# Performance work log

Hardware: AMD Instinct MI355X
Metric: run time of the kernel (lower is better)

Reference implementation:

```python
import jax, jax.numpy as jnp
import numpy as np

B, S, H = 1, 2048, 1024
E, INTER, TOP_K = 8, 2048, 2
ALPHA, LIMIT = 1.702, 7.0


def setup_inputs() -> dict:
    key = jax.random.key(0)
    ks = jax.random.split(key, 7)
    sc = 0.02
    return {
        'hidden_states': jax.random.normal(ks[0], (B, S, H), jnp.float32),
        'router_w': jax.random.normal(ks[1], (H, E), jnp.float32) * sc,
        'router_b': jax.random.normal(ks[2], (E,), jnp.float32) * sc,
        'gate_up_proj': jax.random.normal(ks[3], (E, H, 2 * INTER), jnp.float32) * sc,
        'gate_up_bias': jax.random.normal(ks[4], (E, 2 * INTER), jnp.float32) * sc,
        'down_proj': jax.random.normal(ks[5], (E, INTER, H), jnp.float32) * sc,
        'down_bias': jax.random.normal(ks[6], (E, H), jnp.float32) * sc,
    }


def reference(hidden_states, router_w, router_b, gate_up_proj, gate_up_bias, down_proj, down_bias):
    x = hidden_states  # [B,S,H]
    # router: top-k over expert logits, softmax over selected logits (gpt-oss style)
    logits = jnp.einsum('bsh,he->bse', x, router_w) + router_b
    top_vals, top_idx = jax.lax.top_k(logits, TOP_K)          # [B,S,K]
    topk_weights = jax.nn.softmax(top_vals, axis=-1)          # [B,S,K]
    # dense per-expert gate_up GEMM (dispatch is identity on 1 device)
    gu = jnp.einsum('bsh,ehn->besn', x, gate_up_proj)         # [B,E,S,2I]
    gu = gu + gate_up_bias[None, :, None, :]
    gate = jnp.minimum(gu[..., :INTER], LIMIT)
    up = jnp.clip(gu[..., INTER:], -LIMIT, LIMIT)
    glu = gate * jax.nn.sigmoid(gate * ALPHA)
    act = (up + 1.0) * glu                                    # [B,E,S,I]
    down = jnp.einsum('besl,elh->besh', act, down_proj)       # [B,E,S,H]
    down = down + down_bias[None, :, None, :]
    # combine: gather each token's K selected expert outputs, weight and sum
    down_bseh = jnp.transpose(down, (0, 2, 1, 3))             # [B,S,E,H]
    idx = jnp.broadcast_to(top_idx[..., None], (B, S, TOP_K, H))
    sel = jnp.take_along_axis(down_bseh, idx, axis=2)         # [B,S,K,H]
    return (sel * topk_weights[..., None]).sum(axis=2)        # [B,S,H]
```

## Files before the change

### kernel.cpp

```cpp
#include <hip/hip_runtime.h>
#include <hip/hip_bf16.h>
#include <math.h>

#define S 2048
#define H 1024
#define NE 8
#define INTER 2048
#define ALPHA 1.702f
#define LIMIT 7.0f

typedef __bf16 bf16x8 __attribute__((ext_vector_type(8)));
typedef float f32x4 __attribute__((ext_vector_type(4)));
typedef unsigned short u16x8 __attribute__((ext_vector_type(8)));

#define WS_COUNTS 0
#define WS_SLOTS  4096
#define WS_W      (WS_SLOTS + NE*S*4)
#define WS_XB     (WS_W + 2*S*4)
#define WS_GUP    (WS_XB + (size_t)S*H*2)
#define WS_DPN    (WS_GUP + (size_t)NE*2*INTER*H*2)
#define WS_ACT    (WS_DPN + (size_t)NE*H*INTER*2)

static __device__ __forceinline__ unsigned short f2bf(float f) {
    union { __hip_bfloat16 h; unsigned short u; } cv;
    cv.h = __float2bfloat16(f);
    return cv.u;
}

static __device__ __forceinline__ void gload16(const void* g, void* l) {
    __builtin_amdgcn_global_load_lds(
        (const __attribute__((address_space(1))) unsigned int*)(unsigned long long)g,
        (__attribute__((address_space(3))) unsigned int*)(unsigned int)(unsigned long long)l,
        16, 0, 0);
}

__global__ __launch_bounds__(64) void router_conv(
    const float* __restrict__ x, const float* __restrict__ rw,
    const float* __restrict__ rb, int* __restrict__ counts,
    int* __restrict__ slots, float* __restrict__ slot_w,
    unsigned short* __restrict__ xb)
{
    int tok = blockIdx.x;
    int lane = threadIdx.x;
    const float4* xr = (const float4*)(x + (size_t)tok * H);
    ushort4* xo = (ushort4*)(xb + (size_t)tok * H);
    float acc[NE];
#pragma unroll
    for (int e = 0; e < NE; ++e) acc[e] = 0.f;
#pragma unroll
    for (int p = 0; p < H / 256; ++p) {
        int idx = p * 64 + lane;
        float4 v = xr[idx];
        ushort4 o;
        o.x = f2bf(v.x); o.y = f2bf(v.y); o.z = f2bf(v.z); o.w = f2bf(v.w);
        xo[idx] = o;
        const float* wr = rw + (size_t)idx * 4 * NE;
#pragma unroll
        for (int e = 0; e < NE; ++e)
            acc[e] += v.x * wr[e] + v.y * wr[NE + e] + v.z * wr[2 * NE + e] + v.w * wr[3 * NE + e];
    }
#pragma unroll
    for (int e = 0; e < NE; ++e) {
#pragma unroll
        for (int off = 32; off > 0; off >>= 1)
            acc[e] += __shfl_down(acc[e], off);
    }
    if (lane == 0) {
        float v[NE];
#pragma unroll
        for (int e = 0; e < NE; ++e) v[e] = acc[e] + rb[e];
        int i1 = 0; float v1 = v[0];
#pragma unroll
        for (int e = 1; e < NE; ++e) if (v[e] > v1) { v1 = v[e]; i1 = e; }
        int i2 = -1; float v2 = -3.0e38f;
#pragma unroll
        for (int e = 0; e < NE; ++e) if (e != i1 && v[e] > v2) { v2 = v[e]; i2 = e; }
        float w1 = 1.f / (1.f + expf(v2 - v1));
        float w2 = 1.f - w1;
        int p1 = atomicAdd(&counts[i1], 1);
        slots[i1 * S + p1] = tok * 2;
        slot_w[tok * 2] = w1;
        int p2 = atomicAdd(&counts[i2], 1);
        slots[i2 * S + p2] = tok * 2 + 1;
        slot_w[tok * 2 + 1] = w2;
    }
}

__global__ __launch_bounds__(256) void prep(
    const float* __restrict__ gup, const float* __restrict__ dp,
    unsigned short* __restrict__ gw, unsigned short* __restrict__ dw)
{
    int z = blockIdx.y;
    int e = z / 3, which = z % 3;
    const float* in;
    unsigned short* out;
    int K, N, istride;
    if (which == 0) {
        in = gup + (size_t)e * H * 2 * INTER;
        out = gw + (size_t)e * 2 * INTER * H;
        K = H; N = INTER; istride = 2 * INTER;
    } else if (which == 1) {
        in = gup + (size_t)e * H * 2 * INTER + INTER;
        out = gw + (size_t)e * 2 * INTER * H + (size_t)INTER * H;
        K = H; N = INTER; istride = 2 * INTER;
    } else {
        in = dp + (size_t)e * INTER * H;
        out = dw + (size_t)e * H * INTER;
        K = INTER; N = H; istride = H;
    }
    int ntiles = N / 64;
    int k0 = (blockIdx.x / ntiles) * 64;
    int n0 = (blockIdx.x % ntiles) * 64;

    __shared__ unsigned short tile[64][68];
    int t = threadIdx.x;
    int lk = t >> 4, ln = (t & 15) * 4;
#pragma unroll
    for (int p = 0; p < 4; ++p) {
        int kk = lk + p * 16;
        float4 v = *(const float4*)(in + (size_t)(k0 + kk) * istride + n0 + ln);
        ushort4 o;
        o.x = f2bf(v.x); o.y = f2bf(v.y); o.z = f2bf(v.z); o.w = f2bf(v.w);
        *(ushort4*)&tile[kk][ln] = o;
    }
    __syncthreads();
    int wn = t >> 3, wk = (t & 7) * 8;
#pragma unroll
    for (int p = 0; p < 2; ++p) {
        int nn = wn + p * 32;
        u16x8 o;
#pragma unroll
        for (int i = 0; i < 8; ++i) o[i] = tile[wk + i][nn];
        *(u16x8*)(out + (size_t)(n0 + nn) * K + k0 + wk) = o;
    }
}

__global__ __launch_bounds__(256) void gateup_mfma(
    const unsigned short* __restrict__ xb,
    const unsigned short* __restrict__ gw,
    const float* __restrict__ gub,
    const int* __restrict__ counts, const int* __restrict__ slots,
    unsigned short* __restrict__ act)
{
    int e = blockIdx.z;
    int cnt = counts[e];
    int m0 = blockIdx.y * 128;
    if (m0 >= cnt) return;
    int n0 = blockIdx.x * 64;

    __shared__ unsigned short As[128 * 32];
    __shared__ unsigned short Gs[64 * 32];
    __shared__ unsigned short Us[64 * 32];
    __shared__ int sl[128];

    int t = threadIdx.x;
    int lane = t & 63, w = t >> 6;
    if (t < 128) {
        int r = m0 + t;
        sl[t] = slots[e * S + (r < cnt ? r : cnt - 1)];
    }
    __syncthreads();

    int quad = lane >> 4, l16 = lane & 15;
    int wm = (w >> 1) * 64, wn = (w & 1) * 32;

    int ar0 = w * 32 + (lane >> 2);
    int ar1 = ar0 + 16;
    const unsigned short* ap0 = xb + (size_t)(sl[ar0] >> 1) * H + (lane & 3) * 8;
    const unsigned short* ap1 = xb + (size_t)(sl[ar1] >> 1) * H + (lane & 3) * 8;
    int bn = w * 16 + (lane >> 2);
    const unsigned short* gp = gw + (size_t)e * 2 * INTER * H + (size_t)(n0 + bn) * H + (lane & 3) * 8;
    const unsigned short* up = gp + (size_t)INTER * H;

    unsigned short* la0 = &As[(2 * w) * 512 + lane * 8];
    unsigned short* la1 = &As[(2 * w + 1) * 512 + lane * 8];
    unsigned short* lg = &Gs[w * 512 + lane * 8];
    unsigned short* lu = &Us[w * 512 + lane * 8];

    f32x4 accg[4][2], accu[4][2];
#pragma unroll
    for (int mi = 0; mi < 4; ++mi)
#pragma unroll
        for (int ni = 0; ni < 2; ++ni) {
            accg[mi][ni] = (f32x4){0.f, 0.f, 0.f, 0.f};
            accu[mi][ni] = (f32x4){0.f, 0.f, 0.f, 0.f};
        }

    for (int k0 = 0; k0 < H; k0 += 32) {
        __syncthreads();
        gload16(ap0 + k0, la0);
        gload16(ap1 + k0, la1);
        gload16(gp + k0, lg);
        gload16(up + k0, lu);
        __syncthreads();
        bf16x8 af[4], gf[2], uf[2];
#pragma unroll
        for (int mi = 0; mi < 4; ++mi)
            af[mi] = *(const bf16x8*)&As[(wm + mi * 16 + l16) * 32 + quad * 8];
#pragma unroll
        for (int ni = 0; ni < 2; ++ni) {
            gf[ni] = *(const bf16x8*)&Gs[(wn + ni * 16 + l16) * 32 + quad * 8];
            uf[ni] = *(const bf16x8*)&Us[(wn + ni * 16 + l16) * 32 + quad * 8];
        }
#pragma unroll
        for (int mi = 0; mi < 4; ++mi)
#pragma unroll
            for (int ni = 0; ni < 2; ++ni) {
                accg[mi][ni] = __builtin_amdgcn_mfma_f32_16x16x32_bf16(af[mi], gf[ni], accg[mi][ni], 0, 0, 0);
                accu[mi][ni] = __builtin_amdgcn_mfma_f32_16x16x32_bf16(af[mi], uf[ni], accu[mi][ni], 0, 0, 0);
            }
    }

    const float* gb = gub + (size_t)e * 2 * INTER;
#pragma unroll
    for (int mi = 0; mi < 4; ++mi) {
#pragma unroll
        for (int r = 0; r < 4; ++r) {
            int rt = wm + mi * 16 + quad * 4 + r;
            if (m0 + rt >= cnt) continue;
            int slot = sl[rt];
            unsigned short* orow = act + (size_t)slot * INTER;
#pragma unroll
            for (int ni = 0; ni < 2; ++ni) {
                int col = n0 + wn + ni * 16 + l16;
                float gate = accg[mi][ni][r] + gb[col];
                float uv = accu[mi][ni][r] + gb[INTER + col];
                gate = fminf(gate, LIMIT);
                uv = fminf(fmaxf(uv, -LIMIT), LIMIT);
                float glu = gate / (1.f + __expf(-ALPHA * gate));
                orow[col] = f2bf((uv + 1.f) * glu);
            }
        }
    }
}

__global__ __launch_bounds__(256) void down_mfma(
    const unsigned short* __restrict__ act,
    const unsigned short* __restrict__ dw,
    const float* __restrict__ db,
    const int* __restrict__ counts, const int* __restrict__ slots,
    const float* __restrict__ slot_w,
    float* __restrict__ out)
{
    int e = blockIdx.z >> 1;
    int ks = blockIdx.z & 1;
    int cnt = counts[e];
    int m0 = blockIdx.y * 128;
    if (m0 >= cnt) return;
    int n0 = blockIdx.x * 64;

    __shared__ unsigned short As[128 * 32];
    __shared__ unsigned short Bs[64 * 32];
    __shared__ int sl[128];

    int t = threadIdx.x;
    int lane = t & 63, w = t >> 6;
    if (t < 128) {
        int r = m0 + t;
        sl[t] = slots[e * S + (r < cnt ? r : cnt - 1)];
    }
    __syncthreads();

    int quad = lane >> 4, l16 = lane & 15;
    int wm = (w >> 1) * 64, wn = (w & 1) * 32;

    int ar0 = w * 32 + (lane >> 2);
    int ar1 = ar0 + 16;
    int kbase = ks * (INTER / 2);
    const unsigned short* ap0 = act + (size_t)sl[ar0] * INTER + kbase + (lane & 3) * 8;
    const unsigned short* ap1 = act + (size_t)sl[ar1] * INTER + kbase + (lane & 3) * 8;
    int bn = w * 16 + (lane >> 2);
    const unsigned short* bp = dw + (size_t)e * H * INTER + (size_t)(n0 + bn) * INTER + kbase + (lane & 3) * 8;

    unsigned short* la0 = &As[(2 * w) * 512 + lane * 8];
    unsigned short* la1 = &As[(2 * w + 1) * 512 + lane * 8];
    unsigned short* lb = &Bs[w * 512 + lane * 8];

    f32x4 acc[4][2];
#pragma unroll
    for (int mi = 0; mi < 4; ++mi)
#pragma unroll
        for (int ni = 0; ni < 2; ++ni)
            acc[mi][ni] = (f32x4){0.f, 0.f, 0.f, 0.f};

    for (int k0 = 0; k0 < INTER / 2; k0 += 32) {
        __syncthreads();
        gload16(ap0 + k0, la0);
        gload16(ap1 + k0, la1);
        gload16(bp + k0, lb);
        __syncthreads();
        bf16x8 af[4], bf[2];
#pragma unroll
        for (int mi = 0; mi < 4; ++mi)
            af[mi] = *(const bf16x8*)&As[(wm + mi * 16 + l16) * 32 + quad * 8];
#pragma unroll
        for (int ni = 0; ni < 2; ++ni)
            bf[ni] = *(const bf16x8*)&Bs[(wn + ni * 16 + l16) * 32 + quad * 8];
#pragma unroll
        for (int mi = 0; mi < 4; ++mi)
#pragma unroll
            for (int ni = 0; ni < 2; ++ni)
                acc[mi][ni] = __builtin_amdgcn_mfma_f32_16x16x32_bf16(af[mi], bf[ni], acc[mi][ni], 0, 0, 0);
    }

    const float* dbr = db + (size_t)e * H;
#pragma unroll
    for (int mi = 0; mi < 4; ++mi) {
#pragma unroll
        for (int r = 0; r < 4; ++r) {
            int rt = wm + mi * 16 + quad * 4 + r;
            if (m0 + rt >= cnt) continue;
            int slot = sl[rt];
            int tok = slot >> 1;
            float wgt = slot_w[slot];
#pragma unroll
            for (int ni = 0; ni < 2; ++ni) {
                int col = n0 + wn + ni * 16 + l16;
                float rr = acc[mi][ni][r] + (ks == 0 ? dbr[col] : 0.f);
                atomicAdd(&out[(size_t)tok * H + col], wgt * rr);
            }
        }
    }
}

extern "C" void kernel_launch(void* const* d_in, const int* in_sizes, int n_in,
                              void* d_out, int out_size, void* d_ws, size_t ws_size,
                              hipStream_t stream)
{
    const float* x   = (const float*)d_in[0];
    const float* rw  = (const float*)d_in[1];
    const float* rb  = (const float*)d_in[2];
    const float* gup = (const float*)d_in[3];
    const float* gub = (const float*)d_in[4];
    const float* dp  = (const float*)d_in[5];
    const float* db  = (const float*)d_in[6];
    float* out = (float*)d_out;

    char* ws = (char*)d_ws;
    int* counts            = (int*)(ws + WS_COUNTS);
    int* slots             = (int*)(ws + WS_SLOTS);
    float* slot_w          = (float*)(ws + WS_W);
    unsigned short* xb     = (unsigned short*)(ws + WS_XB);
    unsigned short* gw     = (unsigned short*)(ws + WS_GUP);
    unsigned short* dw     = (unsigned short*)(ws + WS_DPN);
    unsigned short* act    = (unsigned short*)(ws + WS_ACT);

    hipMemsetAsync(counts, 0, 4096, stream);
    hipMemsetAsync(out, 0, (size_t)S * H * sizeof(float), stream);

    router_conv<<<S, 64, 0, stream>>>(x, rw, rb, counts, slots, slot_w, xb);

    prep<<<dim3(512, NE * 3), 256, 0, stream>>>(gup, dp, gw, dw);

    gateup_mfma<<<dim3(INTER / 64, 16, NE), 256, 0, stream>>>(
        xb, gw, gub, counts, slots, act);

    down_mfma<<<dim3(H / 64, 16, NE * 2), 256, 0, stream>>>(
        act, dw, db, counts, slots, slot_w, out);
}
```

Before: 452.9 us.

## Store converted expert weights in K-blocked layout and stream prep over N chunks

The weight conversion kernel now writes bf16 weights as 32-row K blocks with N-major contiguous 32-element rows, so each GEMM K-step reads one contiguous block instead of strided rows. Prep becomes a persistent-per-K-block loop with register double buffering and fp32 LDS transposes, using fewer, larger blocks. Both GEMMs update their B-operand addressing to match. The aim is fully coalesced writes in prep and contiguous B tile loads in the GEMMs, at the cost of fewer prep blocks (768) with serial loops.

```diff
diff --git a/kernel.cpp b/kernel.cpp
--- a/kernel.cpp
+++ b/kernel.cpp
@@ -32,6 +32,11 @@
         (const __attribute__((address_space(1))) unsigned int*)(unsigned long long)g,
         (__attribute__((address_space(3))) unsigned int*)(unsigned int)(unsigned long long)l,
         16, 0, 0);
+}
+
+static __device__ __forceinline__ void ldsbar() {
+    asm volatile("s_waitcnt lgkmcnt(0)" ::: "memory");
+    __builtin_amdgcn_s_barrier();
 }
 
 __global__ __launch_bounds__(64) void router_conv(
@@ -90,48 +95,62 @@
     const float* __restrict__ gup, const float* __restrict__ dp,
     unsigned short* __restrict__ gw, unsigned short* __restrict__ dw)
 {
-    int z = blockIdx.y;
-    int e = z / 3, which = z % 3;
+    int b = blockIdx.x;
     const float* in;
     unsigned short* out;
-    int K, N, istride;
-    if (which == 0) {
-        in = gup + (size_t)e * H * 2 * INTER;
-        out = gw + (size_t)e * 2 * INTER * H;
-        K = H; N = INTER; istride = 2 * INTER;
-    } else if (which == 1) {
-        in = gup + (size_t)e * H * 2 * INTER + INTER;
-        out = gw + (size_t)e * 2 * INTER * H + (size_t)INTER * H;
-        K = H; N = INTER; istride = 2 * INTER;
+    int W, NC;
+    if (b < NE * 32) {
+        int e = b >> 5, kb = b & 31;
+        in  = gup + ((size_t)e * H + kb * 32) * (2 * INTER);
+        out = gw  + (size_t)e * 2 * INTER * H + (size_t)kb * 2 * INTER * 32;
+        W = 2 * INTER; NC = (2 * INTER) / 64;
     } else {
-        in = dp + (size_t)e * INTER * H;
-        out = dw + (size_t)e * H * INTER;
-        K = INTER; N = H; istride = H;
-    }
-    int ntiles = N / 64;
-    int k0 = (blockIdx.x / ntiles) * 64;
-    int n0 = (blockIdx.x % ntiles) * 64;
-
-    __shared__ unsigned short tile[64][68];
+        int bb = b - NE * 32;
+        int e = bb >> 6, kb = bb & 63;
+        in  = dp + ((size_t)e * INTER + kb * 32) * H;
+        out = dw + (size_t)e * INTER * H + (size_t)kb * H * 32;
+        W = H; NC = H / 64;
+    }
+
+    __shared__ float tile[32][65];
     int t = threadIdx.x;
-    int lk = t >> 4, ln = (t & 15) * 4;
-#pragma unroll
-    for (int p = 0; p < 4; ++p) {
-        int kk = lk + p * 16;
-        float4 v = *(const float4*)(in + (size_t)(k0 + kk) * istride + n0 + ln);
-        ushort4 o;
-        o.x = f2bf(v.x); o.y = f2bf(v.y); o.z = f2bf(v.z); o.w = f2bf(v.w);
-        *(ushort4*)&tile[kk][ln] = o;
-    }
-    __syncthreads();
-    int wn = t >> 3, wk = (t & 7) * 8;
-#pragma unroll
-    for (int p = 0; p < 2; ++p) {
-        int nn = wn + p * 32;
-        u16x8 o;
-#pragma unroll
-        for (int i = 0; i < 8; ++i) o[i] = tile[wk + i][nn];
-        *(u16x8*)(out + (size_t)(n0 + nn) * K + k0 + wk) = o;
+    int lk = t >> 3, ln = (t & 7) * 8;
+    int rn = t >> 2, rk = (t & 3) * 8;
+
+    const float* src = in + (size_t)lk * W + ln;
+    float4 a0, a1, b0, b1;
+    a0 = *(const float4*)(src);       a1 = *(const float4*)(src + 4);
+    b0 = *(const float4*)(src + 64);  b1 = *(const float4*)(src + 68);
+
+    for (int nc = 0; nc < NC; nc += 2) {
+        *(f32x4*)&tile[lk][ln]     = (f32x4){a0.x, a0.y, a0.z, a0.w};
+        *(f32x4*)&tile[lk][ln + 4] = (f32x4){a1.x, a1.y, a1.z, a1.w};
+        if (nc + 2 < NC) {
+            const float* s = src + (size_t)(nc + 2) * 64;
+            a0 = *(const float4*)(s); a1 = *(const float4*)(s + 4);
+        }
+        ldsbar();
+        {
+            u16x8 o;
+#pragma unroll
+            for (int i = 0; i < 8; ++i) o[i] = f2bf(tile[rk + i][rn]);
+            *(u16x8*)(out + (size_t)(nc * 64 + rn) * 32 + rk) = o;
+        }
+        ldsbar();
+        *(f32x4*)&tile[lk][ln]     = (f32x4){b0.x, b0.y, b0.z, b0.w};
+        *(f32x4*)&tile[lk][ln + 4] = (f32x4){b1.x, b1.y, b1.z, b1.w};
+        if (nc + 3 < NC) {
+            const float* s = src + (size_t)(nc + 3) * 64;
+            b0 = *(const float4*)(s); b1 = *(const float4*)(s + 4);
+        }
+        ldsbar();
+        {
+            u16x8 o;
+#pragma unroll
+            for (int i = 0; i < 8; ++i) o[i] = f2bf(tile[rk + i][rn]);
+            *(u16x8*)(out + (size_t)((nc + 1) * 64 + rn) * 32 + rk) = o;
+        }
+        ldsbar();
     }
 }
 
@@ -169,8 +188,8 @@
     const unsigned short* ap0 = xb + (size_t)(sl[ar0] >> 1) * H + (lane & 3) * 8;
     const unsigned short* ap1 = xb + (size_t)(sl[ar1] >> 1) * H + (lane & 3) * 8;
     int bn = w * 16 + (lane >> 2);
-    const unsigned short* gp = gw + (size_t)e * 2 * INTER * H + (size_t)(n0 + bn) * H + (lane & 3) * 8;
-    const unsigned short* up = gp + (size_t)INTER * H;
+    const unsigned short* gp = gw + (size_t)e * 2 * INTER * H + (size_t)(n0 + bn) * 32 + (lane & 3) * 8;
+    const unsigned short* up = gp + (size_t)INTER * 32;
 
     unsigned short* la0 = &As[(2 * w) * 512 + lane * 8];
     unsigned short* la1 = &As[(2 * w + 1) * 512 + lane * 8];
@@ -190,8 +209,8 @@
         __syncthreads();
         gload16(ap0 + k0, la0);
         gload16(ap1 + k0, la1);
-        gload16(gp + k0, lg);
-        gload16(up + k0, lu);
+        gload16(gp + (size_t)k0 * 2 * INTER, lg);
+        gload16(up + (size_t)k0 * 2 * INTER, lu);
         __syncthreads();
         bf16x8 af[4], gf[2], uf[2];
 #pragma unroll
@@ -270,7 +289,7 @@
     const unsigned short* ap0 = act + (size_t)sl[ar0] * INTER + kbase + (lane & 3) * 8;
     const unsigned short* ap1 = act + (size_t)sl[ar1] * INTER + kbase + (lane & 3) * 8;
     int bn = w * 16 + (lane >> 2);
-    const unsigned short* bp = dw + (size_t)e * H * INTER + (size_t)(n0 + bn) * INTER + kbase + (lane & 3) * 8;
+    const unsigned short* bp = dw + (size_t)e * H * INTER + (size_t)kbase * H + (size_t)(n0 + bn) * 32 + (lane & 3) * 8;
 
     unsigned short* la0 = &As[(2 * w) * 512 + lane * 8];
     unsigned short* la1 = &As[(2 * w + 1) * 512 + lane * 8];
@@ -287,7 +306,7 @@
         __syncthreads();
         gload16(ap0 + k0, la0);
         gload16(ap1 + k0, la1);
-        gload16(bp + k0, lb);
+        gload16(bp + (size_t)k0 * H, lb);
         __syncthreads();
         bf16x8 af[4], bf[2];
 #pragma unroll
@@ -350,7 +369,7 @@
 
     router_conv<<<S, 64, 0, stream>>>(x, rw, rb, counts, slots, slot_w, xb);
 
-    prep<<<dim3(512, NE * 3), 256, 0, stream>>>(gup, dp, gw, dw);
+    prep<<<NE * 32 + NE * 64, 256, 0, stream>>>(gup, dp, gw, dw);
 
     gateup_mfma<<<dim3(INTER / 64, 16, NE), 256, 0, stream>>>(
         xb, gw, gub, counts, slots, act);
```

After: 475.4 us. 5.0% more time.

## Fuse weight bf16 conversion into GEMM tile loads, drop prep kernel

Applied to the files above, without the earlier changes.

Removes the separate pass that converted and transposed fp32 expert weights to bf16 in workspace. The gate/up and down GEMM kernels now load fp32 weight tiles directly into shared memory and convert them to bf16 while building MFMA fragments. This eliminates a full read and write of all weights, but each block now fetches twice the bytes per weight tile and performs scalar strided LDS reads plus conversions in the inner loop.

```diff
diff --git a/kernel.cpp b/kernel.cpp
--- a/kernel.cpp
+++ b/kernel.cpp
@@ -11,15 +11,12 @@
 
 typedef __bf16 bf16x8 __attribute__((ext_vector_type(8)));
 typedef float f32x4 __attribute__((ext_vector_type(4)));
-typedef unsigned short u16x8 __attribute__((ext_vector_type(8)));
 
 #define WS_COUNTS 0
 #define WS_SLOTS  4096
 #define WS_W      (WS_SLOTS + NE*S*4)
 #define WS_XB     (WS_W + 2*S*4)
-#define WS_GUP    (WS_XB + (size_t)S*H*2)
-#define WS_DPN    (WS_GUP + (size_t)NE*2*INTER*H*2)
-#define WS_ACT    (WS_DPN + (size_t)NE*H*INTER*2)
+#define WS_ACT    (WS_XB + (size_t)S*H*2)
 
 static __device__ __forceinline__ unsigned short f2bf(float f) {
     union { __hip_bfloat16 h; unsigned short u; } cv;
@@ -86,58 +83,9 @@
     }
 }
 
-__global__ __launch_bounds__(256) void prep(
-    const float* __restrict__ gup, const float* __restrict__ dp,
-    unsigned short* __restrict__ gw, unsigned short* __restrict__ dw)
-{
-    int z = blockIdx.y;
-    int e = z / 3, which = z % 3;
-    const float* in;
-    unsigned short* out;
-    int K, N, istride;
-    if (which == 0) {
-        in = gup + (size_t)e * H * 2 * INTER;
-        out = gw + (size_t)e * 2 * INTER * H;
-        K = H; N = INTER; istride = 2 * INTER;
-    } else if (which == 1) {
-        in = gup + (size_t)e * H * 2 * INTER + INTER;
-        out = gw + (size_t)e * 2 * INTER * H + (size_t)INTER * H;
-        K = H; N = INTER; istride = 2 * INTER;
-    } else {
-        in = dp + (size_t)e * INTER * H;
-        out = dw + (size_t)e * H * INTER;
-        K = INTER; N = H; istride = H;
-    }
-    int ntiles = N / 64;
-    int k0 = (blockIdx.x / ntiles) * 64;
-    int n0 = (blockIdx.x % ntiles) * 64;
-
-    __shared__ unsigned short tile[64][68];
-    int t = threadIdx.x;
-    int lk = t >> 4, ln = (t & 15) * 4;
-#pragma unroll
-    for (int p = 0; p < 4; ++p) {
-        int kk = lk + p * 16;
-        float4 v = *(const float4*)(in + (size_t)(k0 + kk) * istride + n0 + ln);
-        ushort4 o;
-        o.x = f2bf(v.x); o.y = f2bf(v.y); o.z = f2bf(v.z); o.w = f2bf(v.w);
-        *(ushort4*)&tile[kk][ln] = o;
-    }
-    __syncthreads();
-    int wn = t >> 3, wk = (t & 7) * 8;
-#pragma unroll
-    for (int p = 0; p < 2; ++p) {
-        int nn = wn + p * 32;
-        u16x8 o;
-#pragma unroll
-        for (int i = 0; i < 8; ++i) o[i] = tile[wk + i][nn];
-        *(u16x8*)(out + (size_t)(n0 + nn) * K + k0 + wk) = o;
-    }
-}
-
 __global__ __launch_bounds__(256) void gateup_mfma(
     const unsigned short* __restrict__ xb,
-    const unsigned short* __restrict__ gw,
+    const float* __restrict__ gup,
     const float* __restrict__ gub,
     const int* __restrict__ counts, const int* __restrict__ slots,
     unsigned short* __restrict__ act)
@@ -149,8 +97,8 @@
     int n0 = blockIdx.x * 64;
 
     __shared__ unsigned short As[128 * 32];
-    __shared__ unsigned short Gs[64 * 32];
-    __shared__ unsigned short Us[64 * 32];
+    __shared__ float Gs[32][64];
+    __shared__ float Us[32][64];
     __shared__ int sl[128];
 
     int t = threadIdx.x;
@@ -168,14 +116,17 @@
     int ar1 = ar0 + 16;
     const unsigned short* ap0 = xb + (size_t)(sl[ar0] >> 1) * H + (lane & 3) * 8;
     const unsigned short* ap1 = xb + (size_t)(sl[ar1] >> 1) * H + (lane & 3) * 8;
-    int bn = w * 16 + (lane >> 2);
-    const unsigned short* gp = gw + (size_t)e * 2 * INTER * H + (size_t)(n0 + bn) * H + (lane & 3) * 8;
-    const unsigned short* up = gp + (size_t)INTER * H;
-
     unsigned short* la0 = &As[(2 * w) * 512 + lane * 8];
     unsigned short* la1 = &As[(2 * w + 1) * 512 + lane * 8];
-    unsigned short* lg = &Gs[w * 512 + lane * 8];
-    unsigned short* lu = &Us[w * 512 + lane * 8];
+
+    int brow = t >> 4;
+    int bcol = (t & 15) * 4;
+    const float* gsrc = gup + (size_t)e * H * 2 * INTER
+                      + (size_t)brow * (2 * INTER) + n0 + bcol;
+    const float* usrc = gsrc + INTER;
+    float* lg = &Gs[brow][bcol];
+    float* lu = &Us[brow][bcol];
+    const size_t rs16 = (size_t)16 * 2 * INTER;
 
     f32x4 accg[4][2], accu[4][2];
 #pragma unroll
@@ -190,17 +141,29 @@
         __syncthreads();
         gload16(ap0 + k0, la0);
         gload16(ap1 + k0, la1);
-        gload16(gp + k0, lg);
-        gload16(up + k0, lu);
+        const float* gk = gsrc + (size_t)k0 * 2 * INTER;
+        const float* uk = usrc + (size_t)k0 * 2 * INTER;
+        gload16(gk, lg);
+        gload16(gk + rs16, (char*)lg + 4096);
+        gload16(uk, lu);
+        gload16(uk + rs16, (char*)lu + 4096);
         __syncthreads();
+
         bf16x8 af[4], gf[2], uf[2];
 #pragma unroll
         for (int mi = 0; mi < 4; ++mi)
             af[mi] = *(const bf16x8*)&As[(wm + mi * 16 + l16) * 32 + quad * 8];
 #pragma unroll
         for (int ni = 0; ni < 2; ++ni) {
-            gf[ni] = *(const bf16x8*)&Gs[(wn + ni * 16 + l16) * 32 + quad * 8];
-            uf[ni] = *(const bf16x8*)&Us[(wn + ni * 16 + l16) * 32 + quad * 8];
+            int n = wn + ni * 16 + l16;
+            union { bf16x8 v; __bf16 e[8]; } ug, uu;
+#pragma unroll
+            for (int i = 0; i < 8; ++i) {
+                ug.e[i] = (__bf16)Gs[quad * 8 + i][n];
+                uu.e[i] = (__bf16)Us[quad * 8 + i][n];
+            }
+            gf[ni] = ug.v;
+            uf[ni] = uu.v;
         }
 #pragma unroll
         for (int mi = 0; mi < 4; ++mi)
@@ -236,7 +199,7 @@
 
 __global__ __launch_bounds__(256) void down_mfma(
     const unsigned short* __restrict__ act,
-    const unsigned short* __restrict__ dw,
+    const float* __restrict__ dp,
     const float* __restrict__ db,
     const int* __restrict__ counts, const int* __restrict__ slots,
     const float* __restrict__ slot_w,
@@ -250,7 +213,7 @@
     int n0 = blockIdx.x * 64;
 
     __shared__ unsigned short As[128 * 32];
-    __shared__ unsigned short Bs[64 * 32];
+    __shared__ float Bs[32][64];
     __shared__ int sl[128];
 
     int t = threadIdx.x;
@@ -269,12 +232,15 @@
     int kbase = ks * (INTER / 2);
     const unsigned short* ap0 = act + (size_t)sl[ar0] * INTER + kbase + (lane & 3) * 8;
     const unsigned short* ap1 = act + (size_t)sl[ar1] * INTER + kbase + (lane & 3) * 8;
-    int bn = w * 16 + (lane >> 2);
-    const unsigned short* bp = dw + (size_t)e * H * INTER + (size_t)(n0 + bn) * INTER + kbase + (lane & 3) * 8;
-
     unsigned short* la0 = &As[(2 * w) * 512 + lane * 8];
     unsigned short* la1 = &As[(2 * w + 1) * 512 + lane * 8];
-    unsigned short* lb = &Bs[w * 512 + lane * 8];
+
+    int brow = t >> 4;
+    int bcol = (t & 15) * 4;
+    const float* bsrc = dp + (size_t)e * INTER * H
+                      + (size_t)(kbase + brow) * H + n0 + bcol;
+    float* lb = &Bs[brow][bcol];
+    const size_t rs16 = (size_t)16 * H;
 
     f32x4 acc[4][2];
 #pragma unroll
@@ -287,15 +253,24 @@
         __syncthreads();
         gload16(ap0 + k0, la0);
         gload16(ap1 + k0, la1);
-        gload16(bp + k0, lb);
+        const float* bk = bsrc + (size_t)k0 * H;
+        gload16(bk, lb);
+        gload16(bk + rs16, (char*)lb + 4096);
         __syncthreads();
+
         bf16x8 af[4], bf[2];
 #pragma unroll
         for (int mi = 0; mi < 4; ++mi)
             af[mi] = *(const bf16x8*)&As[(wm + mi * 16 + l16) * 32 + quad * 8];
 #pragma unroll
-        for (int ni = 0; ni < 2; ++ni)
-            bf[ni] = *(const bf16x8*)&Bs[(wn + ni * 16 + l16) * 32 + quad * 8];
+        for (int ni = 0; ni < 2; ++ni) {
+            int n = wn + ni * 16 + l16;
+            union { bf16x8 v; __bf16 e[8]; } ub;
+#pragma unroll
+            for (int i = 0; i < 8; ++i)
+                ub.e[i] = (__bf16)Bs[quad * 8 + i][n];
+            bf[ni] = ub.v;
+        }
 #pragma unroll
         for (int mi = 0; mi < 4; ++mi)
 #pragma unroll
@@ -341,8 +316,6 @@
     int* slots             = (int*)(ws + WS_SLOTS);
     float* slot_w          = (float*)(ws + WS_W);
     unsigned short* xb     = (unsigned short*)(ws + WS_XB);
-    unsigned short* gw     = (unsigned short*)(ws + WS_GUP);
-    unsigned short* dw     = (unsigned short*)(ws + WS_DPN);
     unsigned short* act    = (unsigned short*)(ws + WS_ACT);
 
     hipMemsetAsync(counts, 0, 4096, stream);
@@ -350,11 +323,9 @@
 
     router_conv<<<S, 64, 0, stream>>>(x, rw, rb, counts, slots, slot_w, xb);
 
-    prep<<<dim3(512, NE * 3), 256, 0, stream>>>(gup, dp, gw, dw);
-
     gateup_mfma<<<dim3(INTER / 64, 16, NE), 256, 0, stream>>>(
-        xb, gw, gub, counts, slots, act);
+        xb, gup, gub, counts, slots, act);
 
     down_mfma<<<dim3(H / 64, 16, NE * 2), 256, 0, stream>>>(
-        act, dw, db, counts, slots, slot_w, out);
-}
+        act, dp, db, counts, slots, slot_w, out);
+}
```

Result: faster. 438.8 us (-3.1%).
